# Kernel tuning notes

Measured on AMD Instinct MI355X. Metric: run time of the kernel, lower is better.

## Reference

```python
import jax, jax.numpy as jnp
import numpy as np

B, L, D, H = 8, 2048, 1024, 16  # batch, max_len, n_embd, n_head


def setup_inputs() -> dict:
    key = jax.random.key(0)
    k1, k2, k3 = jax.random.split(key, 3)
    x = jax.random.normal(k1, (B, L, D), dtype=jnp.float32)
    # learned per-head position-mixing weight (n_heads, out_features, in_features)
    W = jax.random.normal(k2, (H, L, L), dtype=jnp.float32) * 0.02
    W_proj = jax.random.normal(k3, (D, D), dtype=jnp.float32) * 0.02
    b_proj = jnp.zeros((D,), dtype=jnp.float32)
    return {"x": x, "W": W, "W_proj": W_proj, "b_proj": b_proj}


def reference(x, W, W_proj, b_proj):
    Bb, Ll, Dd = x.shape
    d = Dd // H
    xi = x.reshape(Bb, Ll, H, d)
    # tril mask multiplies the weight (zeros above diagonal, NOT -inf),
    # then softmax over the last (input-position) axis — faithful to torch code.
    mask = jnp.tril(jnp.ones((Ll, Ll), dtype=W.dtype))
    normalized_weight = jax.nn.softmax(W * mask, axis=-1)  # (H, L, L)
    # position mixing: out position i gathers over input positions l per head
    mixed = jnp.einsum('blhd,hil->bihd', xi, normalized_weight)
    mixed = mixed.reshape(Bb, Ll, Dd)
    # c_proj (dropout is identity at p=0.0 / eval)
    return mixed @ W_proj.T + b_proj
```

## Files before the change

kernel.cpp:

```cpp
#include <hip/hip_runtime.h>
#include <hip/hip_bf16.h>

#define BB 8
#define LL 2048
#define DD 1024
#define HH 16
#define HD 64
#define NMIX 512

typedef float  f32x4  __attribute__((ext_vector_type(4)));
typedef short  bf16x8 __attribute__((ext_vector_type(8)));
typedef short  s8v    __attribute__((ext_vector_type(8)));
typedef short  s4v    __attribute__((ext_vector_type(4)));

typedef unsigned int u32;
typedef const __attribute__((address_space(1))) u32* gas_ptr;
typedef __attribute__((address_space(3))) u32* las_ptr;

static __device__ __forceinline__ void gload16(const void* g, void* l) {
    __builtin_amdgcn_global_load_lds((gas_ptr)g, (las_ptr)l, 16, 0, 0);
}

static __device__ __forceinline__ short f2bf(float f) {
    union { float f; u32 u; } a; a.f = f;
    u32 r = a.u + 0x7FFFu + ((a.u >> 16) & 1u);
    return (short)(r >> 16);
}

__global__ __launch_bounds__(256) void softmax_kernel(const float* __restrict__ W,
                                                      short* __restrict__ NW) {
    const int row = blockIdx.x;
    const int i = row & (LL - 1);
    const float* Wr = W + (size_t)row * LL;
    const int tid = threadIdx.x;
    const int lane = tid & 63, wave = tid >> 6;
    const int jbase = tid * 8;

    float4 a = ((const float4*)Wr)[2 * tid];
    float4 b = ((const float4*)Wr)[2 * tid + 1];
    float v[8] = {a.x, a.y, a.z, a.w, b.x, b.y, b.z, b.w};
#pragma unroll
    for (int j = 0; j < 8; ++j)
        if (jbase + j > i) v[j] = 0.f;

    float mx = v[0];
#pragma unroll
    for (int j = 1; j < 8; ++j) mx = fmaxf(mx, v[j]);
#pragma unroll
    for (int off = 32; off; off >>= 1) mx = fmaxf(mx, __shfl_xor(mx, off));

    __shared__ float redmax[4], redsum[4];
    if (lane == 0) redmax[wave] = mx;
    __syncthreads();
    mx = fmaxf(fmaxf(redmax[0], redmax[1]), fmaxf(redmax[2], redmax[3]));

    float s = 0.f;
#pragma unroll
    for (int j = 0; j < 8; ++j) { v[j] = __expf(v[j] - mx); s += v[j]; }
#pragma unroll
    for (int off = 32; off; off >>= 1) s += __shfl_xor(s, off);
    if (lane == 0) redsum[wave] = s;
    __syncthreads();
    s = redsum[0] + redsum[1] + redsum[2] + redsum[3];
    const float inv = 1.f / s;

    s8v o;
#pragma unroll
    for (int j = 0; j < 8; ++j) o[j] = f2bf(v[j] * inv);
    *(s8v*)(NW + (size_t)row * LL + jbase) = o;
}

__global__ __launch_bounds__(256) void transpose_x(const float* __restrict__ x,
                                                   short* __restrict__ xT) {
    const int hb = blockIdx.z;
    const int h = hb >> 3, b = hb & 7;
    const int l0 = blockIdx.x * 32, d0 = blockIdx.y * 32;
    const int tx = threadIdx.x, ty = threadIdx.y;

    __shared__ float tile[32][33];
#pragma unroll
    for (int j = 0; j < 4; ++j) {
        int l = l0 + ty + 8 * j;
        tile[ty + 8 * j][tx] = x[((size_t)(b * LL + l)) * DD + h * HD + d0 + tx];
    }
    __syncthreads();
#pragma unroll
    for (int j = 0; j < 4; ++j) {
        int n = b * HD + d0 + ty + 8 * j;
        xT[((size_t)(h * NMIX + n)) * LL + l0 + tx] = f2bf(tile[tx][ty + 8 * j]);
    }
}

__global__ __launch_bounds__(256) void cvt_wproj(const float* __restrict__ Wp,
                                                 short* __restrict__ WpB) {
    const int idx = (blockIdx.x * 256 + threadIdx.x) * 4;
    float4 v = *(const float4*)&Wp[idx];
    s4v o = { f2bf(v.x), f2bf(v.y), f2bf(v.z), f2bf(v.w) };
    *(s4v*)&WpB[idx] = o;
}

__global__ __launch_bounds__(256) void gemm_mix(const short* __restrict__ NW,
                                                const short* __restrict__ xT,
                                                short* __restrict__ mixed) {
    constexpr int K = LL;
    const int h = blockIdx.z;
    const short* A  = NW + (size_t)h * LL * LL;
    const short* BT = xT + (size_t)h * NMIX * LL;
    const int row0 = blockIdx.x * 128;
    const int col0 = blockIdx.y * 128;

    __shared__ short sA[128 * 32];
    __shared__ short sB[128 * 32];

    const int tid = threadIdx.x;
    const int wave = tid >> 6, lane = tid & 63;
    const int fr = lane & 15, fq = lane >> 4;
    const int wr = wave >> 1, wc = wave & 1;
    const int srow = lane >> 2;
    const int scol = (lane & 3) * 8;

    f32x4 acc[4][4];
#pragma unroll
    for (int m = 0; m < 4; ++m)
#pragma unroll
        for (int n = 0; n < 4; ++n)
            acc[m][n] = f32x4{0.f, 0.f, 0.f, 0.f};

    for (int k0 = 0; k0 < K; k0 += 32) {
#pragma unroll
        for (int q = 0; q < 2; ++q) {
            const int sseg = q * 4 + wave;
            const short* ga = A  + (size_t)(row0 + sseg * 16 + srow) * K + k0 + scol;
            const short* gb = BT + (size_t)(col0 + sseg * 16 + srow) * K + k0 + scol;
            gload16(ga, &sA[sseg * 512]);
            gload16(gb, &sB[sseg * 512]);
        }
        __syncthreads();
        bf16x8 af[4], bfv[4];
#pragma unroll
        for (int m = 0; m < 4; ++m)
            af[m] = *(const bf16x8*)&sA[(wr * 64 + m * 16 + fr) * 32 + fq * 8];
#pragma unroll
        for (int n = 0; n < 4; ++n)
            bfv[n] = *(const bf16x8*)&sB[(wc * 64 + n * 16 + fr) * 32 + fq * 8];
#pragma unroll
        for (int m = 0; m < 4; ++m)
#pragma unroll
            for (int n = 0; n < 4; ++n)
                acc[m][n] = __builtin_amdgcn_mfma_f32_16x16x32_bf16(af[m], bfv[n], acc[m][n], 0, 0, 0);
        __syncthreads();
    }

    const int hbase = h * HD;
#pragma unroll
    for (int m = 0; m < 4; ++m) {
        const int gi = row0 + wr * 64 + m * 16 + fq * 4;
#pragma unroll
        for (int n = 0; n < 4; ++n) {
            const int ng = col0 + wc * 64 + n * 16 + fr;
            const int bb = ng >> 6, dd = ng & 63;
            const size_t base = ((size_t)(bb * LL) + gi) * DD + hbase + dd;
#pragma unroll
            for (int r = 0; r < 4; ++r)
                mixed[base + (size_t)r * DD] = f2bf(acc[m][n][r]);
        }
    }
}

__global__ __launch_bounds__(256) void gemm_proj(const short* __restrict__ Amix,
                                                 const short* __restrict__ WpB,
                                                 const float* __restrict__ bias,
                                                 float* __restrict__ out) {
    constexpr int K = DD;
    const int row0 = blockIdx.x * 128;
    const int col0 = blockIdx.y * 128;

    __shared__ short sA[128 * 32];
    __shared__ short sB[128 * 32];

    const int tid = threadIdx.x;
    const int wave = tid >> 6, lane = tid & 63;
    const int fr = lane & 15, fq = lane >> 4;
    const int wr = wave >> 1, wc = wave & 1;
    const int srow = lane >> 2;
    const int scol = (lane & 3) * 8;

    f32x4 acc[4][4];
#pragma unroll
    for (int m = 0; m < 4; ++m)
#pragma unroll
        for (int n = 0; n < 4; ++n)
            acc[m][n] = f32x4{0.f, 0.f, 0.f, 0.f};

    for (int k0 = 0; k0 < K; k0 += 32) {
#pragma unroll
        for (int q = 0; q < 2; ++q) {
            const int sseg = q * 4 + wave;
            const short* ga = Amix + (size_t)(row0 + sseg * 16 + srow) * K + k0 + scol;
            const short* gb = WpB  + (size_t)(col0 + sseg * 16 + srow) * K + k0 + scol;
            gload16(ga, &sA[sseg * 512]);
            gload16(gb, &sB[sseg * 512]);
        }
        __syncthreads();
        bf16x8 af[4], bfv[4];
#pragma unroll
        for (int m = 0; m < 4; ++m)
            af[m] = *(const bf16x8*)&sA[(wr * 64 + m * 16 + fr) * 32 + fq * 8];
#pragma unroll
        for (int n = 0; n < 4; ++n)
            bfv[n] = *(const bf16x8*)&sB[(wc * 64 + n * 16 + fr) * 32 + fq * 8];
#pragma unroll
        for (int m = 0; m < 4; ++m)
#pragma unroll
            for (int n = 0; n < 4; ++n)
                acc[m][n] = __builtin_amdgcn_mfma_f32_16x16x32_bf16(af[m], bfv[n], acc[m][n], 0, 0, 0);
        __syncthreads();
    }

#pragma unroll
    for (int m = 0; m < 4; ++m) {
        const int grow = row0 + wr * 64 + m * 16 + fq * 4;
#pragma unroll
        for (int n = 0; n < 4; ++n) {
            const int gcol = col0 + wc * 64 + n * 16 + fr;
            const float bj = bias[gcol];
#pragma unroll
            for (int r = 0; r < 4; ++r)
                out[(size_t)(grow + r) * DD + gcol] = acc[m][n][r] + bj;
        }
    }
}

extern "C" void kernel_launch(void* const* d_in, const int* in_sizes, int n_in,
                              void* d_out, int out_size, void* d_ws, size_t ws_size,
                              hipStream_t stream) {
    const float* x  = (const float*)d_in[0];
    const float* W  = (const float*)d_in[1];
    const float* Wp = (const float*)d_in[2];
    const float* bp = (const float*)d_in[3];
    float* out = (float*)d_out;

    char* ws = (char*)d_ws;
    short* NW    = (short*)(ws);
    short* xT    = (short*)(ws + 134217728);
    short* mixed = (short*)(ws + 167772160);
    short* WpB   = (short*)(ws + 201326592);

    softmax_kernel<<<HH * LL, 256, 0, stream>>>(W, NW);
    transpose_x<<<dim3(LL / 32, HD / 32, HH * BB), dim3(32, 8), 0, stream>>>(x, xT);
    cvt_wproj<<<1024, 256, 0, stream>>>(Wp, WpB);
    gemm_mix<<<dim3(LL / 128, NMIX / 128, HH), 256, 0, stream>>>(NW, xT, mixed);
    gemm_proj<<<dim3((BB * LL) / 128, DD / 128), 256, 0, stream>>>(mixed, WpB, bp, out);
}
```

Before: 624.8 us.

## Use wave-per-row softmax and XCD-aware block swizzle in both GEMMs

The softmax kernel now assigns one 64-lane wave per row, with four rows per block. Each lane holds 32 values, so the max and sum reductions need only wave shuffles, with no shared memory and no __syncthreads. Both GEMM kernels remap the flat block index so that consecutive logical tiles land on the same XCD, since the hardware dispatches blocks round-robin across 8 XCDs. This is meant to improve L2 reuse of the shared A/B panels. The costs are higher register pressure in softmax and a swizzle that hardcodes the grid sizes.

```diff
diff --git a/kernel.cpp b/kernel.cpp
--- a/kernel.cpp
+++ b/kernel.cpp
@@ -29,45 +29,49 @@
 
 __global__ __launch_bounds__(256) void softmax_kernel(const float* __restrict__ W,
                                                       short* __restrict__ NW) {
-    const int row = blockIdx.x;
+    const int wave = threadIdx.x >> 6, lane = threadIdx.x & 63;
+    const int row = blockIdx.x * 4 + wave;
     const int i = row & (LL - 1);
-    const float* Wr = W + (size_t)row * LL;
-    const int tid = threadIdx.x;
-    const int lane = tid & 63, wave = tid >> 6;
-    const int jbase = tid * 8;
-
-    float4 a = ((const float4*)Wr)[2 * tid];
-    float4 b = ((const float4*)Wr)[2 * tid + 1];
-    float v[8] = {a.x, a.y, a.z, a.w, b.x, b.y, b.z, b.w};
-#pragma unroll
-    for (int j = 0; j < 8; ++j)
-        if (jbase + j > i) v[j] = 0.f;
+    const float4* Wr = (const float4*)(W + (size_t)row * LL);
+
+    float4 c[8];
+#pragma unroll
+    for (int j = 0; j < 8; ++j) c[j] = Wr[j * 64 + lane];
+
+    float v[32];
+#pragma unroll
+    for (int j = 0; j < 8; ++j) {
+        v[4 * j + 0] = c[j].x; v[4 * j + 1] = c[j].y;
+        v[4 * j + 2] = c[j].z; v[4 * j + 3] = c[j].w;
+    }
+#pragma unroll
+    for (int j = 0; j < 8; ++j) {
+        const int e = (j * 64 + lane) * 4;
+#pragma unroll
+        for (int k = 0; k < 4; ++k)
+            if (e + k > i) v[4 * j + k] = 0.f;
+    }
 
     float mx = v[0];
 #pragma unroll
-    for (int j = 1; j < 8; ++j) mx = fmaxf(mx, v[j]);
+    for (int t = 1; t < 32; ++t) mx = fmaxf(mx, v[t]);
 #pragma unroll
     for (int off = 32; off; off >>= 1) mx = fmaxf(mx, __shfl_xor(mx, off));
 
-    __shared__ float redmax[4], redsum[4];
-    if (lane == 0) redmax[wave] = mx;
-    __syncthreads();
-    mx = fmaxf(fmaxf(redmax[0], redmax[1]), fmaxf(redmax[2], redmax[3]));
-
     float s = 0.f;
 #pragma unroll
-    for (int j = 0; j < 8; ++j) { v[j] = __expf(v[j] - mx); s += v[j]; }
+    for (int t = 0; t < 32; ++t) { v[t] = __expf(v[t] - mx); s += v[t]; }
 #pragma unroll
     for (int off = 32; off; off >>= 1) s += __shfl_xor(s, off);
-    if (lane == 0) redsum[wave] = s;
-    __syncthreads();
-    s = redsum[0] + redsum[1] + redsum[2] + redsum[3];
     const float inv = 1.f / s;
 
-    s8v o;
-#pragma unroll
-    for (int j = 0; j < 8; ++j) o[j] = f2bf(v[j] * inv);
-    *(s8v*)(NW + (size_t)row * LL + jbase) = o;
+    short* orow = NW + (size_t)row * LL;
+#pragma unroll
+    for (int j = 0; j < 8; ++j) {
+        s4v o = { f2bf(v[4 * j + 0] * inv), f2bf(v[4 * j + 1] * inv),
+                  f2bf(v[4 * j + 2] * inv), f2bf(v[4 * j + 3] * inv) };
+        *(s4v*)(orow + (j * 64 + lane) * 4) = o;
+    }
 }
 
 __global__ __launch_bounds__(256) void transpose_x(const float* __restrict__ x,
@@ -103,11 +107,15 @@
                                                 const short* __restrict__ xT,
                                                 short* __restrict__ mixed) {
     constexpr int K = LL;
-    const int h = blockIdx.z;
+    const u32 flat = blockIdx.x + 16u * (blockIdx.y + 4u * blockIdx.z);
+    const u32 swz = (flat & 7u) * 128u + (flat >> 3);
+    const int rb = (int)(swz & 15u);
+    const int cb = (int)((swz >> 4) & 3u);
+    const int h  = (int)(swz >> 6);
     const short* A  = NW + (size_t)h * LL * LL;
     const short* BT = xT + (size_t)h * NMIX * LL;
-    const int row0 = blockIdx.x * 128;
-    const int col0 = blockIdx.y * 128;
+    const int row0 = rb * 128;
+    const int col0 = cb * 128;
 
     __shared__ short sA[128 * 32];
     __shared__ short sB[128 * 32];
@@ -172,8 +180,10 @@
                                                  const float* __restrict__ bias,
                                                  float* __restrict__ out) {
     constexpr int K = DD;
-    const int row0 = blockIdx.x * 128;
-    const int col0 = blockIdx.y * 128;
+    const u32 flat = blockIdx.x + 128u * blockIdx.y;
+    const u32 swz = (flat & 7u) * 128u + (flat >> 3);
+    const int row0 = (int)(swz & 127u) * 128;
+    const int col0 = (int)(swz >> 7) * 128;
 
     __shared__ short sA[128 * 32];
     __shared__ short sB[128 * 32];
@@ -246,7 +256,7 @@
     short* mixed = (short*)(ws + 167772160);
     short* WpB   = (short*)(ws + 201326592);
 
-    softmax_kernel<<<HH * LL, 256, 0, stream>>>(W, NW);
+    softmax_kernel<<<HH * LL / 4, 256, 0, stream>>>(W, NW);
     transpose_x<<<dim3(LL / 32, HD / 32, HH * BB), dim3(32, 8), 0, stream>>>(x, xT);
     cvt_wproj<<<1024, 256, 0, stream>>>(Wp, WpB);
     gemm_mix<<<dim3(LL / 128, NMIX / 128, HH), 256, 0, stream>>>(NW, xT, mixed);
```

New measurement: 611.4 us. -2.2%, faster.
